# Performance work log

Measured on AMD Instinct MI355X. Metric: run time of the kernel, lower is better.

Reference implementation:

```python
import jax, jax.numpy as jnp
import numpy as np

B, C_IN, T, C_OUT, K = 32, 1024, 512, 1024, 3


def conv1d(x, w, b, stride, pad):
    # x: (B, Cin, L), w: (Cout, Cin, K)
    y = jax.lax.conv_general_dilated(
        x, w, window_strides=(stride,), padding=[(pad, pad)],
        dimension_numbers=("NCH", "OIH", "NCH"))
    return y + b[None, :, None]


def setup_inputs() -> dict:
    key = jax.random.key(0)
    k1, k2, k3, k4, k5 = jax.random.split(key, 5)
    inputs = jax.random.normal(k1, (B, C_IN, T), dtype=jnp.float32)
    # offset conv is zero-initialized in the module; use small random values
    # so the deformable path is actually exercised.
    w_off = jax.random.normal(k2, (K, C_IN, K), dtype=jnp.float32) * 0.01
    b_off = jax.random.normal(k3, (K,), dtype=jnp.float32) * 0.01
    w_conv = jax.random.normal(k4, (C_OUT, C_IN, K), dtype=jnp.float32) * (1.0 / np.sqrt(C_IN * K))
    b_conv = jax.random.normal(k5, (C_OUT,), dtype=jnp.float32) * 0.01
    return {"inputs": inputs, "w_off": w_off, "b_off": b_off,
            "w_conv": w_conv, "b_conv": b_conv}


def _forward(inputs, w_off, b_off, w_conv, b_conv):
    Bb, C, Tt = inputs.shape
    Kk = w_off.shape[0]
    half = Kk // 2
    H, W = Tt, C  # grid_sample view: (B, 1, H=T, W=C)

    # offset prediction conv (stride 1, padding K//2) -> (B, K, T) -> (B, T, K)
    offsets = conv1d(inputs, w_off, b_off, 1, half)
    pred = jnp.transpose(offsets, (0, 2, 1))  # (B, H, K)

    # normalized y grid (align_corners=True style normalization, as in _make_grid)
    pos = jnp.arange(-half, half + 1, dtype=jnp.float32)  # (K,)
    base = (jnp.arange(H, dtype=jnp.float32) / (H - 1)) * 2.0 - 1.0  # (H,)
    g = base[None, :, None] + pos[None, None, :] * (2.0 / (H - 1)) + pred  # (B,H,K)
    g = jnp.clip(g, -1.0, 1.0)

    # F.grid_sample default align_corners=False: pixel = ((g+1)*size - 1)/2
    py = ((g + 1.0) * H - 1.0) * 0.5  # (B, H, K)
    y0 = jnp.floor(py)
    ty = py - y0
    y0i = y0.astype(jnp.int32)
    y0c = jnp.clip(y0i, 0, H - 1)      # border padding
    y1c = jnp.clip(y0i + 1, 0, H - 1)

    # x grid is data-independent: w_grid = w/(W-1)*2-1, so pixel_x = w*W/(W-1)-0.5
    wj = jnp.arange(W, dtype=jnp.float32)
    px = wj * (W / (W - 1.0)) - 0.5
    x0 = jnp.floor(px)
    tx = px - x0
    x0i = x0.astype(jnp.int32)
    x0c = jnp.clip(x0i, 0, W - 1)
    x1c = jnp.clip(x0i + 1, 0, W - 1)

    A = jnp.transpose(inputs, (0, 2, 1))  # (B, H, W)
    # separable bilinear: mix along W first (offset only shifts y)
    xmix = (1.0 - tx)[None, None, :] * A[:, :, x0c] + tx[None, None, :] * A[:, :, x1c]  # (B,H,W)

    b_ix = jnp.arange(Bb)[:, None, None]
    g0 = xmix[b_ix, y0c]  # (B, H, K, W)
    g1 = xmix[b_ix, y1c]  # (B, H, K, W)
    sampled = (1.0 - ty)[..., None] * g0 + ty[..., None] * g1  # (B, H, K, W)

    # final conv over kernel axis: (B*H, W=C_in, K) -> (B, H, C_out)
    out = jnp.einsum("bhkw,owk->bho", sampled, w_conv) + b_conv[None, None, :]
    return out


def reference(inputs, w_off, b_off, w_conv, b_conv):
    return _forward(inputs, w_off, b_off, w_conv, b_conv)
```

## Files before the change

kernel.cpp:

```cpp
#include <hip/hip_runtime.h>

#define NB 32
#define NC 1024
#define NT 512
#define NO 1024
#define KTILES 48

typedef __attribute__((ext_vector_type(8))) short bf16x8;
typedef __attribute__((ext_vector_type(4))) float f32x4;

#define FENCE asm volatile("" ::: "memory")
#define BAR do{ FENCE; __builtin_amdgcn_s_barrier(); FENCE; }while(0)
#define LGKM0 asm volatile("s_waitcnt lgkmcnt(0)" ::: "memory")

__device__ __forceinline__ unsigned short f2bf(float f){
  unsigned int i = __float_as_uint(f);
  i += 0x7fffu + ((i >> 16) & 1u);
  return (unsigned short)(i >> 16);
}

__device__ __forceinline__ unsigned int blend_pack(unsigned int u0, unsigned int u1, float t){
  float a0 = __uint_as_float(u0 << 16);
  float a1 = __uint_as_float(u0 & 0xffff0000u);
  float b0 = __uint_as_float(u1 << 16);
  float b1 = __uint_as_float(u1 & 0xffff0000u);
  float r0 = fmaf(t, b0 - a0, a0);
  float r1 = fmaf(t, b1 - a1, a1);
  return (unsigned int)f2bf(r0) | (((unsigned int)f2bf(r1)) << 16);
}

__device__ __forceinline__ void async16(const void* g, void* l){
  __builtin_amdgcn_global_load_lds((const __attribute__((address_space(1))) void*)g,
                                   (__attribute__((address_space(3))) void*)l, 16, 0, 0);
}

__global__ __launch_bounds__(256) void transpose_off_kernel(const float* __restrict__ x,
    const float* __restrict__ w_off, unsigned short* __restrict__ atr,
    float* __restrict__ part){
  __shared__ float tile[64][67];
  __shared__ float wsh[64][9];
  __shared__ float red[4][64][3];
  int b = blockIdx.z, c0 = blockIdx.y * 64, t0 = blockIdx.x * 64;
  int tx = threadIdx.x & 63, wy = threadIdx.x >> 6;
  const float* xp = x + ((size_t)b * NC + c0) * NT + t0;
  #pragma unroll
  for (int i = 0; i < 16; i++){ int cl = wy * 16 + i; tile[cl][1 + tx] = xp[(size_t)cl * NT + tx]; }
  if (threadIdx.x < 64){
    tile[tx][0]  = (t0 > 0)       ? xp[(size_t)tx * NT - 1]  : 0.f;
  } else if (threadIdx.x < 128){
    tile[tx][65] = (t0 + 64 < NT) ? xp[(size_t)tx * NT + 64] : 0.f;
  }
  for (int i = threadIdx.x; i < 576; i += 256){
    int c = i / 9, r = i % 9;
    wsh[c][r] = w_off[(size_t)(r / 3) * 3072 + (size_t)(c0 + c) * 3 + (r % 3)];
  }
  __syncthreads();
  int p = threadIdx.x & 31, r2 = threadIdx.x >> 5;
  unsigned int* dst = (unsigned int*)(atr + ((size_t)b * NT + t0) * NC + c0);
  #pragma unroll
  for (int i = 0; i < 8; i++){
    int tl = r2 * 8 + i;
    unsigned int lo = f2bf(tile[2 * p][1 + tl]);
    unsigned int hi = f2bf(tile[2 * p + 1][1 + tl]);
    dst[(size_t)tl * (NC / 2) + p] = lo | (hi << 16);
  }
  float s0 = 0.f, s1 = 0.f, s2 = 0.f;
  #pragma unroll 4
  for (int i = 0; i < 16; i++){
    int c = wy * 16 + i;
    float xm = tile[c][tx], xc = tile[c][1 + tx], xq = tile[c][2 + tx];
    s0 += xm * wsh[c][0] + xc * wsh[c][1] + xq * wsh[c][2];
    s1 += xm * wsh[c][3] + xc * wsh[c][4] + xq * wsh[c][5];
    s2 += xm * wsh[c][6] + xc * wsh[c][7] + xq * wsh[c][8];
  }
  red[wy][tx][0] = s0; red[wy][tx][1] = s1; red[wy][tx][2] = s2;
  __syncthreads();
  if (threadIdx.x < 192){
    int tl = threadIdx.x & 63, o = threadIdx.x >> 6;
    float v = red[0][tl][o] + red[1][tl][o] + red[2][tl][o] + red[3][tl][o];
    size_t m = (size_t)b * NT + t0 + tl;
    part[(m * 3 + o) * 16 + blockIdx.y] = v;
  }
}

__global__ __launch_bounds__(256) void wmix_kernel(const float* __restrict__ w_conv,
                                                   unsigned short* __restrict__ wm2){
  int gid = blockIdx.x * 256 + threadIdx.x;
  int o = gid >> 10, c = gid & 1023;
  const float ratio = (float)(1024.0 / 1023.0);
  float acc0 = 0.f, acc1 = 0.f, acc2 = 0.f;
  int wlo = (c > 2) ? c - 2 : 0;
  int whi = (c < 1021) ? c + 2 : 1023;
  for (int w = wlo; w <= whi; ++w){
    float px = (float)w * ratio - 0.5f;
    float x0 = floorf(px);
    float tx = px - x0;
    int i0 = (int)x0;
    int i0c = min(max(i0, 0), 1023);
    int i1c = min(max(i0 + 1, 0), 1023);
    float s = ((i0c == c) ? (1.0f - tx) : 0.f) + ((i1c == c) ? tx : 0.f);
    if (s != 0.f){
      const float* wc = w_conv + ((size_t)o * 1024 + w) * 3;
      acc0 += s * wc[0]; acc1 += s * wc[1]; acc2 += s * wc[2];
    }
  }
  size_t base = (size_t)o * 3072 + c;
  wm2[base]        = f2bf(acc0);
  wm2[base + 1024] = f2bf(acc1);
  wm2[base + 2048] = f2bf(acc2);
}

__global__ __launch_bounds__(256) void blend_kernel(
    const unsigned short* __restrict__ atr, const float* __restrict__ part,
    const float* __restrict__ b_off, unsigned short* __restrict__ Abl){
  __shared__ int si0[2][3], si1[2][3];
  __shared__ float sty[2][3];
  int row0 = blockIdx.x * 2;
  if (threadIdx.x < 6){
    int lr = (int)threadIdx.x / 3, o = (int)threadIdx.x % 3;
    int row = row0 + lr;
    int gid = row * 3 + o;
    const float* pp = part + (size_t)gid * 16;
    float p = b_off[o];
    #pragma unroll
    for (int i = 0; i < 16; i++) p += pp[i];
    int tt = row & 511;
    float base = (float)tt / 511.0f * 2.0f - 1.0f;
    float g = base + (float)(o - 1) * (float)(2.0 / 511.0) + p;
    g = fminf(1.0f, fmaxf(-1.0f, g));
    float py = ((g + 1.0f) * 512.0f - 1.0f) * 0.5f;
    float y0 = floorf(py);
    int i0 = (int)y0;
    si0[lr][o] = min(max(i0, 0), NT - 1);
    si1[lr][o] = min(max(i0 + 1, 0), NT - 1);
    sty[lr][o] = py - y0;
  }
  __syncthreads();
  int lr = threadIdx.x >> 7;
  int row = row0 + lr;
  int seg = threadIdx.x & 127;
  int b = row >> 9;
  const unsigned short* base = atr + (size_t)b * NT * NC;
  unsigned short* orow = Abl + (size_t)row * 3072 + (size_t)seg * 8;
  uint4 v0[3], v1[3]; float t[3];
  #pragma unroll
  for (int k = 0; k < 3; k++){
    v0[k] = *(const uint4*)(base + (size_t)si0[lr][k] * NC + (size_t)seg * 8);
    v1[k] = *(const uint4*)(base + (size_t)si1[lr][k] * NC + (size_t)seg * 8);
    t[k] = sty[lr][k];
  }
  #pragma unroll
  for (int k = 0; k < 3; k++){
    uint4 rv;
    rv.x = blend_pack(v0[k].x, v1[k].x, t[k]);
    rv.y = blend_pack(v0[k].y, v1[k].y, t[k]);
    rv.z = blend_pack(v0[k].z, v1[k].z, t[k]);
    rv.w = blend_pack(v0[k].w, v1[k].w, t[k]);
    *(uint4*)(orow + k * 1024) = rv;
  }
}

__device__ __forceinline__ void stage_half(const unsigned short* __restrict__ src,
                                           unsigned short* Lbase, int row0, int q,
                                           int w, int lane){
  int l3 = lane >> 3, l7 = lane & 7;
  int swc = ((l7 ^ l3) << 3);
  #pragma unroll
  for (int i = 0; i < 2; i++){
    int ci = i * 8 + w;
    const unsigned short* g = src + (size_t)(row0 + ci * 8 + l3) * 3072 + q * 64 + swc;
    async16(g, Lbase + ci * 512);
  }
}

__global__ __launch_bounds__(512, 2) void gemm8_kernel(
    const unsigned short* __restrict__ A, const unsigned short* __restrict__ Bw,
    const float* __restrict__ b_conv, float* __restrict__ out){
  __shared__ __align__(16) unsigned short L[65536];

  int wg = blockIdx.x;
  int swz = (wg & 7) * 32 + (wg >> 3);
  int mtile = swz >> 2, ntile = swz & 3;
  int m0 = mtile * 256, n0 = ntile * 256;
  int tid = threadIdx.x, lane = tid & 63, w = tid >> 6;
  int wm_ = w >> 2, wn_ = w & 3;
  int lq = lane & 15, q4 = lane >> 4;
  int sl0 = (q4 ^ (lq & 7)) << 3;
  int sl1 = ((4 + q4) ^ (lq & 7)) << 3;
  int hb = wn_ >> 1, nb = (wn_ & 1) * 64;

  f32x4 acc[8][4];
  #pragma unroll
  for (int i = 0; i < 8; i++)
    #pragma unroll
    for (int j = 0; j < 4; j++) acc[i][j] = (f32x4){0.f, 0.f, 0.f, 0.f};

  stage_half(A,  &L[0],                 m0,       0, w, lane);
  stage_half(A,  &L[8192],              m0 + 128, 0, w, lane);
  stage_half(Bw, &L[16384],             n0,       0, w, lane);
  stage_half(Bw, &L[16384 + 8192],      n0 + 128, 0, w, lane);
  stage_half(Bw, &L[32768 + 16384],        n0,       1, w, lane);
  stage_half(Bw, &L[32768 + 16384 + 8192], n0 + 128, 1, w, lane);
  asm volatile("s_waitcnt vmcnt(4)" ::: "memory");
  BAR;

  bf16x8 aA[4][2], bB[4][2];

  for (int t = 0; t < KTILES; ++t){
    int c = (t & 1) * 32768;
    int cn = ((t + 1) & 1) * 32768;
    const unsigned short* LA = &L[c + wm_ * 8192];
    const unsigned short* LB = &L[c + 16384 + hb * 8192];

    #pragma unroll
    for (int mf = 0; mf < 4; mf++){
      int r = mf * 16 + lq;
      aA[mf][0] = *(const bf16x8*)&LA[r * 64 + sl0];
      aA[mf][1] = *(const bf16x8*)&LA[r * 64 + sl1];
    }
    #pragma unroll
    for (int nf = 0; nf < 2; nf++){
      int r = nb + nf * 16 + lq;
      bB[nf][0] = *(const bf16x8*)&LB[r * 64 + sl0];
      bB[nf][1] = *(const bf16x8*)&LB[r * 64 + sl1];
    }
    if (t + 1 < KTILES) stage_half(A, &L[cn], m0, t + 1, w, lane);
    BAR; LGKM0;
    __builtin_amdgcn_s_setprio(1);
    #pragma unroll
    for (int mf = 0; mf < 4; mf++)
      #pragma unroll
      for (int nf = 0; nf < 2; nf++){
        acc[mf][nf] = __builtin_amdgcn_mfma_f32_16x16x32_bf16(aA[mf][0], bB[nf][0], acc[mf][nf], 0, 0, 0);
        acc[mf][nf] = __builtin_amdgcn_mfma_f32_16x16x32_bf16(aA[mf][1], bB[nf][1], acc[mf][nf], 0, 0, 0);
      }
    __builtin_amdgcn_s_setprio(0);
    BAR;

    #pragma unroll
    for (int nf = 2; nf < 4; nf++){
      int r = nb + nf * 16 + lq;
      bB[nf][0] = *(const bf16x8*)&LB[r * 64 + sl0];
      bB[nf][1] = *(const bf16x8*)&LB[r * 64 + sl1];
    }
    if (t + 1 < KTILES) stage_half(A, &L[cn + 8192], m0 + 128, t + 1, w, lane);
    BAR; LGKM0;
    __builtin_amdgcn_s_setprio(1);
    #pragma unroll
    for (int mf = 0; mf < 4; mf++)
      #pragma unroll
      for (int nf = 2; nf < 4; nf++){
        acc[mf][nf] = __builtin_amdgcn_mfma_f32_16x16x32_bf16(aA[mf][0], bB[nf][0], acc[mf][nf], 0, 0, 0);
        acc[mf][nf] = __builtin_amdgcn_mfma_f32_16x16x32_bf16(aA[mf][1], bB[nf][1], acc[mf][nf], 0, 0, 0);
      }
    __builtin_amdgcn_s_setprio(0);
    BAR;

    #pragma unroll
    for (int mf = 0; mf < 4; mf++){
      int r = 64 + mf * 16 + lq;
      aA[mf][0] = *(const bf16x8*)&LA[r * 64 + sl0];
      aA[mf][1] = *(const bf16x8*)&LA[r * 64 + sl1];
    }
    if (t + 2 < KTILES) stage_half(Bw, &L[c + 16384], n0, t + 2, w, lane);
    BAR; LGKM0;
    __builtin_amdgcn_s_setprio(1);
    #pragma unroll
    for (int mf = 0; mf < 4; mf++)
      #pragma unroll
      for (int nf = 2; nf < 4; nf++){
        acc[4 + mf][nf] = __builtin_amdgcn_mfma_f32_16x16x32_bf16(aA[mf][0], bB[nf][0], acc[4 + mf][nf], 0, 0, 0);
        acc[4 + mf][nf] = __builtin_amdgcn_mfma_f32_16x16x32_bf16(aA[mf][1], bB[nf][1], acc[4 + mf][nf], 0, 0, 0);
      }
    __builtin_amdgcn_s_setprio(0);
    BAR;

    if (t + 2 < KTILES) stage_half(Bw, &L[c + 16384 + 8192], n0 + 128, t + 2, w, lane);
    BAR;
    __builtin_amdgcn_s_setprio(1);
    #pragma unroll
    for (int mf = 0; mf < 4; mf++)
      #pragma unroll
      for (int nf = 0; nf < 2; nf++){
        acc[4 + mf][nf] = __builtin_amdgcn_mfma_f32_16x16x32_bf16(aA[mf][0], bB[nf][0], acc[4 + mf][nf], 0, 0, 0);
        acc[4 + mf][nf] = __builtin_amdgcn_mfma_f32_16x16x32_bf16(aA[mf][1], bB[nf][1], acc[4 + mf][nf], 0, 0, 0);
      }
    __builtin_amdgcn_s_setprio(0);
    if (t + 2 < KTILES)      { asm volatile("s_waitcnt vmcnt(4)" ::: "memory"); }
    else if (t + 1 < KTILES) { asm volatile("s_waitcnt vmcnt(0)" ::: "memory"); }
    BAR;
  }

  #pragma unroll
  for (int nf = 0; nf < 4; nf++){
    int n = n0 + wn_ * 64 + nf * 16 + lq;
    float bc = b_conv[n];
    #pragma unroll
    for (int mh = 0; mh < 2; mh++)
      #pragma unroll
      for (int mf = 0; mf < 4; mf++){
        int mr = m0 + wm_ * 128 + mh * 64 + mf * 16 + q4 * 4;
        f32x4 v = acc[mh * 4 + mf][nf];
        #pragma unroll
        for (int j = 0; j < 4; j++)
          out[(size_t)(mr + j) * NO + n] = v[j] + bc;
      }
  }
}

extern "C" void kernel_launch(void* const* d_in, const int* in_sizes, int n_in,
                              void* d_out, int out_size, void* d_ws, size_t ws_size,
                              hipStream_t stream){
  (void)in_sizes; (void)n_in; (void)out_size; (void)ws_size;
  const float* x      = (const float*)d_in[0];
  const float* w_off  = (const float*)d_in[1];
  const float* b_off  = (const float*)d_in[2];
  const float* w_conv = (const float*)d_in[3];
  const float* b_conv = (const float*)d_in[4];
  float* out = (float*)d_out;

  char* ws = (char*)d_ws;
  unsigned short* atr = (unsigned short*)ws;
  float* part = (float*)(ws + 33554432);
  unsigned short* wm2 = (unsigned short*)(ws + 37289984);
  unsigned short* Abl = (unsigned short*)(ws + 43581440);

  hipLaunchKernelGGL(transpose_off_kernel, dim3(NT / 64, NC / 64, NB), dim3(256), 0, stream,
                     x, w_off, atr, part);
  hipLaunchKernelGGL(wmix_kernel,  dim3((1024 * 1024) / 256), dim3(256), 0, stream, w_conv, wm2);
  hipLaunchKernelGGL(blend_kernel, dim3(16384 / 2), dim3(256), 0, stream,
                     atr, part, b_off, Abl);
  hipLaunchKernelGGL(gemm8_kernel, dim3((16384 / 256) * (1024 / 256)), dim3(512), 0, stream,
                     Abl, wm2, b_conv, out);
}
```

Before: 164.3 us.

## Merge prep kernels into one launch and stage GEMM epilogue through LDS

Combines the transpose/offset-conv kernel and the weight-mixing kernel into a single launch, choosing the branch by block index, which removes one launch and lets the two independent jobs overlap. The GEMM epilogue now writes each accumulator fragment into a per-wave LDS tile and reads it back so every lane stores a 16-byte vector to consecutive output columns, replacing scattered 4-byte stores. This adds LDS traffic and waits in the epilogue, and it relies on the reused LDS region no longer being needed by the main loop.

```diff
diff --git a/kernel.cpp b/kernel.cpp
--- a/kernel.cpp
+++ b/kernel.cpp
@@ -34,80 +34,82 @@
                                    (__attribute__((address_space(3))) void*)l, 16, 0, 0);
 }
 
-__global__ __launch_bounds__(256) void transpose_off_kernel(const float* __restrict__ x,
-    const float* __restrict__ w_off, unsigned short* __restrict__ atr,
-    float* __restrict__ part){
+__global__ __launch_bounds__(256) void prep_kernel(const float* __restrict__ x,
+    const float* __restrict__ w_off, const float* __restrict__ w_conv,
+    unsigned short* __restrict__ atr, float* __restrict__ part,
+    unsigned short* __restrict__ wm2){
   __shared__ float tile[64][67];
   __shared__ float wsh[64][9];
   __shared__ float red[4][64][3];
-  int b = blockIdx.z, c0 = blockIdx.y * 64, t0 = blockIdx.x * 64;
-  int tx = threadIdx.x & 63, wy = threadIdx.x >> 6;
-  const float* xp = x + ((size_t)b * NC + c0) * NT + t0;
-  #pragma unroll
-  for (int i = 0; i < 16; i++){ int cl = wy * 16 + i; tile[cl][1 + tx] = xp[(size_t)cl * NT + tx]; }
-  if (threadIdx.x < 64){
-    tile[tx][0]  = (t0 > 0)       ? xp[(size_t)tx * NT - 1]  : 0.f;
-  } else if (threadIdx.x < 128){
-    tile[tx][65] = (t0 + 64 < NT) ? xp[(size_t)tx * NT + 64] : 0.f;
-  }
-  for (int i = threadIdx.x; i < 576; i += 256){
-    int c = i / 9, r = i % 9;
-    wsh[c][r] = w_off[(size_t)(r / 3) * 3072 + (size_t)(c0 + c) * 3 + (r % 3)];
-  }
-  __syncthreads();
-  int p = threadIdx.x & 31, r2 = threadIdx.x >> 5;
-  unsigned int* dst = (unsigned int*)(atr + ((size_t)b * NT + t0) * NC + c0);
-  #pragma unroll
-  for (int i = 0; i < 8; i++){
-    int tl = r2 * 8 + i;
-    unsigned int lo = f2bf(tile[2 * p][1 + tl]);
-    unsigned int hi = f2bf(tile[2 * p + 1][1 + tl]);
-    dst[(size_t)tl * (NC / 2) + p] = lo | (hi << 16);
-  }
-  float s0 = 0.f, s1 = 0.f, s2 = 0.f;
-  #pragma unroll 4
-  for (int i = 0; i < 16; i++){
-    int c = wy * 16 + i;
-    float xm = tile[c][tx], xc = tile[c][1 + tx], xq = tile[c][2 + tx];
-    s0 += xm * wsh[c][0] + xc * wsh[c][1] + xq * wsh[c][2];
-    s1 += xm * wsh[c][3] + xc * wsh[c][4] + xq * wsh[c][5];
-    s2 += xm * wsh[c][6] + xc * wsh[c][7] + xq * wsh[c][8];
-  }
-  red[wy][tx][0] = s0; red[wy][tx][1] = s1; red[wy][tx][2] = s2;
-  __syncthreads();
-  if (threadIdx.x < 192){
-    int tl = threadIdx.x & 63, o = threadIdx.x >> 6;
-    float v = red[0][tl][o] + red[1][tl][o] + red[2][tl][o] + red[3][tl][o];
-    size_t m = (size_t)b * NT + t0 + tl;
-    part[(m * 3 + o) * 16 + blockIdx.y] = v;
-  }
-}
-
-__global__ __launch_bounds__(256) void wmix_kernel(const float* __restrict__ w_conv,
-                                                   unsigned short* __restrict__ wm2){
-  int gid = blockIdx.x * 256 + threadIdx.x;
-  int o = gid >> 10, c = gid & 1023;
-  const float ratio = (float)(1024.0 / 1023.0);
-  float acc0 = 0.f, acc1 = 0.f, acc2 = 0.f;
-  int wlo = (c > 2) ? c - 2 : 0;
-  int whi = (c < 1021) ? c + 2 : 1023;
-  for (int w = wlo; w <= whi; ++w){
-    float px = (float)w * ratio - 0.5f;
-    float x0 = floorf(px);
-    float tx = px - x0;
-    int i0 = (int)x0;
-    int i0c = min(max(i0, 0), 1023);
-    int i1c = min(max(i0 + 1, 0), 1023);
-    float s = ((i0c == c) ? (1.0f - tx) : 0.f) + ((i1c == c) ? tx : 0.f);
-    if (s != 0.f){
-      const float* wc = w_conv + ((size_t)o * 1024 + w) * 3;
-      acc0 += s * wc[0]; acc1 += s * wc[1]; acc2 += s * wc[2];
-    }
-  }
-  size_t base = (size_t)o * 3072 + c;
-  wm2[base]        = f2bf(acc0);
-  wm2[base + 1024] = f2bf(acc1);
-  wm2[base + 2048] = f2bf(acc2);
+  int bid = blockIdx.x;
+  if (bid < 4096){
+    int bx = bid & 7, by = (bid >> 3) & 15, bz = bid >> 7;
+    int b = bz, c0 = by * 64, t0 = bx * 64;
+    int tx = threadIdx.x & 63, wy = threadIdx.x >> 6;
+    const float* xp = x + ((size_t)b * NC + c0) * NT + t0;
+    #pragma unroll
+    for (int i = 0; i < 16; i++){ int cl = wy * 16 + i; tile[cl][1 + tx] = xp[(size_t)cl * NT + tx]; }
+    if (threadIdx.x < 64){
+      tile[tx][0]  = (t0 > 0)       ? xp[(size_t)tx * NT - 1]  : 0.f;
+    } else if (threadIdx.x < 128){
+      tile[tx][65] = (t0 + 64 < NT) ? xp[(size_t)tx * NT + 64] : 0.f;
+    }
+    for (int i = threadIdx.x; i < 576; i += 256){
+      int c = i / 9, r = i % 9;
+      wsh[c][r] = w_off[(size_t)(r / 3) * 3072 + (size_t)(c0 + c) * 3 + (r % 3)];
+    }
+    __syncthreads();
+    int p = threadIdx.x & 31, r2 = threadIdx.x >> 5;
+    unsigned int* dst = (unsigned int*)(atr + ((size_t)b * NT + t0) * NC + c0);
+    #pragma unroll
+    for (int i = 0; i < 8; i++){
+      int tl = r2 * 8 + i;
+      unsigned int lo = f2bf(tile[2 * p][1 + tl]);
+      unsigned int hi = f2bf(tile[2 * p + 1][1 + tl]);
+      dst[(size_t)tl * (NC / 2) + p] = lo | (hi << 16);
+    }
+    float s0 = 0.f, s1 = 0.f, s2 = 0.f;
+    #pragma unroll 4
+    for (int i = 0; i < 16; i++){
+      int c = wy * 16 + i;
+      float xm = tile[c][tx], xc = tile[c][1 + tx], xq = tile[c][2 + tx];
+      s0 += xm * wsh[c][0] + xc * wsh[c][1] + xq * wsh[c][2];
+      s1 += xm * wsh[c][3] + xc * wsh[c][4] + xq * wsh[c][5];
+      s2 += xm * wsh[c][6] + xc * wsh[c][7] + xq * wsh[c][8];
+    }
+    red[wy][tx][0] = s0; red[wy][tx][1] = s1; red[wy][tx][2] = s2;
+    __syncthreads();
+    if (threadIdx.x < 192){
+      int tl = threadIdx.x & 63, o = threadIdx.x >> 6;
+      float v = red[0][tl][o] + red[1][tl][o] + red[2][tl][o] + red[3][tl][o];
+      size_t m = (size_t)b * NT + t0 + tl;
+      part[(m * 3 + o) * 16 + by] = v;
+    }
+  } else {
+    int gid = (bid - 4096) * 256 + threadIdx.x;
+    int o = gid >> 10, c = gid & 1023;
+    const float ratio = (float)(1024.0 / 1023.0);
+    float acc0 = 0.f, acc1 = 0.f, acc2 = 0.f;
+    int wlo = (c > 2) ? c - 2 : 0;
+    int whi = (c < 1021) ? c + 2 : 1023;
+    for (int w = wlo; w <= whi; ++w){
+      float px = (float)w * ratio - 0.5f;
+      float x0 = floorf(px);
+      float tx = px - x0;
+      int i0 = (int)x0;
+      int i0c = min(max(i0, 0), 1023);
+      int i1c = min(max(i0 + 1, 0), 1023);
+      float s = ((i0c == c) ? (1.0f - tx) : 0.f) + ((i1c == c) ? tx : 0.f);
+      if (s != 0.f){
+        const float* wc = w_conv + ((size_t)o * 1024 + w) * 3;
+        acc0 += s * wc[0]; acc1 += s * wc[1]; acc2 += s * wc[2];
+      }
+    }
+    size_t base = (size_t)o * 3072 + c;
+    wm2[base]        = f2bf(acc0);
+    wm2[base + 1024] = f2bf(acc1);
+    wm2[base + 2048] = f2bf(acc2);
+  }
 }
 
 __global__ __launch_bounds__(256) void blend_kernel(
@@ -291,19 +293,32 @@
     BAR;
   }
 
-  #pragma unroll
-  for (int nf = 0; nf < 4; nf++){
-    int n = n0 + wn_ * 64 + nf * 16 + lq;
-    float bc = b_conv[n];
+  {
+    float* Lf = (float*)L;
+    float* wt = Lf + w * 1088;
+    float bcv[4];
+    #pragma unroll
+    for (int nf = 0; nf < 4; nf++) bcv[nf] = b_conv[n0 + wn_ * 64 + nf * 16 + lq];
+    int ncol = n0 + wn_ * 64 + lq * 4;
     #pragma unroll
     for (int mh = 0; mh < 2; mh++)
       #pragma unroll
       for (int mf = 0; mf < 4; mf++){
-        int mr = m0 + wm_ * 128 + mh * 64 + mf * 16 + q4 * 4;
-        f32x4 v = acc[mh * 4 + mf][nf];
         #pragma unroll
-        for (int j = 0; j < 4; j++)
-          out[(size_t)(mr + j) * NO + n] = v[j] + bc;
+        for (int nf = 0; nf < 4; nf++){
+          f32x4 v = acc[mh * 4 + mf][nf];
+          #pragma unroll
+          for (int j = 0; j < 4; j++)
+            wt[(q4 * 4 + j) * 68 + nf * 16 + lq] = v[j] + bcv[nf];
+        }
+        LGKM0;
+        int mrow0 = m0 + wm_ * 128 + mh * 64 + mf * 16;
+        #pragma unroll
+        for (int r = 0; r < 4; r++){
+          f32x4 v = *(const f32x4*)&wt[(r * 4 + q4) * 68 + lq * 4];
+          *(f32x4*)&out[(size_t)(mrow0 + r * 4 + q4) * NO + ncol] = v;
+        }
+        LGKM0;
       }
   }
 }
@@ -325,9 +340,8 @@
   unsigned short* wm2 = (unsigned short*)(ws + 37289984);
   unsigned short* Abl = (unsigned short*)(ws + 43581440);
 
-  hipLaunchKernelGGL(transpose_off_kernel, dim3(NT / 64, NC / 64, NB), dim3(256), 0, stream,
-                     x, w_off, atr, part);
-  hipLaunchKernelGGL(wmix_kernel,  dim3((1024 * 1024) / 256), dim3(256), 0, stream, w_conv, wm2);
+  hipLaunchKernelGGL(prep_kernel,  dim3(8192), dim3(256), 0, stream,
+                     x, w_off, w_conv, atr, part, wm2);
   hipLaunchKernelGGL(blend_kernel, dim3(16384 / 2), dim3(256), 0, stream,
                      atr, part, b_off, Abl);
   hipLaunchKernelGGL(gemm8_kernel, dim3((16384 / 256) * (1024 / 256)), dim3(512), 0, stream,
```

New measurement: 159.3 us, median of 2. 1.03x faster.
